# Kernel optimization log

Measured on AMD Instinct MI355X. Metric: run time of the kernel, lower is better.

Reference implementation:

```python
import jax, jax.numpy as jnp
import numpy as np

EPSILON = 0.1
NITER = 50


def _sinkhorn_transport(cost, epsilon, niter):
    # Faithful to the torch loop: kernel uses exp(-cost/eps), scalings have +100
    # damping, early-exit when both u,v L2 diffs < 0.01 (emulated via a done flag
    # inside a fixed-length scan so it is jit- and vjp-friendly).
    exp_term = jnp.exp(-cost / epsilon)              # [N, M]
    N, M = cost.shape
    u0 = jnp.ones((N, 1), cost.dtype)
    v0 = jnp.ones((M, 1), cost.dtype)

    def step(carry, _):
        u, v, pu, pv, done = carry
        nu = 1.0 / (exp_term @ v + 100.0)            # [N,1]
        nv = 1.0 / (exp_term.T @ nu + 100.0)         # [M,1]
        conv = (jnp.linalg.norm(nu - pu) < 0.01) & (jnp.linalg.norm(nv - pv) < 0.01)
        u_n = jnp.where(done, u, nu)
        v_n = jnp.where(done, v, nv)
        # torch updates prev only when the break was NOT taken this iteration
        pu_n = jnp.where(done | conv, pu, nu)
        pv_n = jnp.where(done | conv, pv, nv)
        return (u_n, v_n, pu_n, pv_n, done | conv), None

    (u, v, _, _, _), _ = jax.lax.scan(step, (u0, v0, u0, v0, jnp.array(False)), None, length=niter)
    # NOTE: original code uses exp(-cost * eps) here (not /eps); keep it faithful.
    return jnp.exp(-cost * epsilon) * u * v.T        # [N, M]


def _interp_lastdim(text, W):
    # PyTorch trilinear interpolate from (1,1,N) -> (D,H,W), align_corners=False.
    # Size-1 depth/height dims reduce to broadcast; only last dim is linear.
    B, C, N = text.shape
    scale = N / W
    x = jnp.maximum((jnp.arange(W, dtype=text.dtype) + 0.5) * scale - 0.5, 0.0)
    x0 = jnp.clip(jnp.floor(x).astype(jnp.int32), 0, N - 1)
    x1 = jnp.minimum(x0 + 1, N - 1)
    w = x - x0.astype(text.dtype)
    return text[:, :, x0] * (1.0 - w) + text[:, :, x1] * w   # [B, C, W]


def _forward(text, image, w1, b1, w2, b2):
    B, C, N = text.shape
    _, _, D, H, W = image.shape
    M = D * H * W
    tf = text.reshape(B * C, N)                      # [L, N]
    imf = image.reshape(B * C, M)                    # [L, M]
    A = tf.T                                         # [N, L]
    Bm = imf.T                                       # [M, L]
    d2 = (jnp.sum(A * A, axis=1)[:, None]
          + jnp.sum(Bm * Bm, axis=1)[None, :]
          - 2.0 * (A @ Bm.T))
    cost = jnp.sqrt(jnp.maximum(d2, 0.0))            # torch.cdist p=2, [N, M]
    T = _sinkhorn_transport(cost, EPSILON, NITER)
    aligned_text = (imf @ T.T).reshape(B, C, N)      # [B, C, N]

    t_line = _interp_lastdim(aligned_text, W)        # [B, C, W]
    t_rs = jnp.broadcast_to(t_line[:, :, None, None, :], (B, C, D, H, W))
    fused = jnp.concatenate([t_rs, image], axis=1)   # [B, 2C, D, H, W]

    h = jnp.einsum('oi,bidhw->bodhw', w1, fused) + b1[None, :, None, None, None]
    h = jax.nn.relu(h)
    g = jnp.einsum('oi,bidhw->bodhw', w2, h) + b2[None, :, None, None, None]
    gate = jax.nn.sigmoid(g)
    return image * (1.0 - gate) + t_rs * gate


def setup_inputs() -> dict:
    key = jax.random.key(0)
    ks = jax.random.split(key, 6)
    B, C, N = 2, 64, 256
    D, H, W = 32, 64, 64
    return {
        'text': jax.random.normal(ks[0], (B, C, N), dtype=jnp.float32),
        'image': jax.random.normal(ks[1], (B, C, D, H, W), dtype=jnp.float32),
        'w1': jax.random.normal(ks[2], (C, 2 * C), dtype=jnp.float32) * (1.0 / np.sqrt(2 * C)),
        'b1': jax.random.normal(ks[3], (C,), dtype=jnp.float32) * 0.01,
        'w2': jax.random.normal(ks[4], (C, C), dtype=jnp.float32) * (1.0 / np.sqrt(C)),
        'b2': jax.random.normal(ks[5], (C,), dtype=jnp.float32) * 0.01,
    }


def reference(text, image, w1, b1, w2, b2):
    return _forward(text, image, w1, b1, w2, b2)
```

## Files before the change

### kernel.cpp

```cpp
#include <hip/hip_runtime.h>

#define L_ 128
#define N_ 256
#define M_ 131072

using short8  = __attribute__((ext_vector_type(8)))  short;
using floatx16 = __attribute__((ext_vector_type(16))) float;

__device__ __forceinline__ unsigned short f2bf(float f) {
  unsigned u = __float_as_uint(f);
  u += 0x7fffu + ((u >> 16) & 1u);
  return (unsigned short)(u >> 16);
}
__device__ __forceinline__ float bf2f(unsigned short s) {
  return __uint_as_float(((unsigned)s) << 16);
}
__device__ __forceinline__ unsigned pack2(float x, float y) {
  return ((unsigned)f2bf(y) << 16) | (unsigned)f2bf(x);
}
__device__ __forceinline__ floatx16 mm(uint4 a, uint4 b, floatx16 c) {
  return __builtin_amdgcn_mfma_f32_32x32x16_bf16(
      __builtin_bit_cast(short8, a), __builtin_bit_cast(short8, b), c, 0, 0, 0);
}

__global__ __launch_bounds__(256, 2) void k_gemm(
    const float* __restrict__ image, const float* __restrict__ text,
    unsigned* __restrict__ imf_Tp, unsigned short* __restrict__ pbuf) {
  __shared__ unsigned SH[13952];
  float* SHf = (float*)SH;
  unsigned* v1 = SH;
  unsigned* uu = SH + 4608;
  unsigned short* w16 = (unsigned short*)(SH + 8960);
  const int t = threadIdx.x;
  const int lane = t & 63, w = t >> 6;
  const int q = lane >> 5, r = lane & 31;
  const int wnu = w >> 1, wm = w & 1;
  const int wl = w >> 1, wn = w & 1;
  const int m_base = blockIdx.x * 256;

  {
    const int nuh = t & 127, half = t >> 7;
    const int n = 4 * (nuh >> 1) + 1 + (nuh & 1);
    float sq = 0.f;
#pragma unroll 8
    for (int j = 0; j < 32; ++j) {
      const int l0 = half * 64 + 2 * j;
      const float x = text[l0 * N_ + n];
      const float y = text[(l0 + 1) * N_ + n];
      sq = fmaf(x, x, fmaf(y, y, sq));
      SH[nuh * 64 + half * 32 + j] = pack2(x, y);
    }
    ((float*)w16)[nuh * 2 + half] = sq;
  }
  __syncthreads();
  uint4 at[2][8];
#pragma unroll
  for (int nt = 0; nt < 2; ++nt)
#pragma unroll
    for (int kk = 0; kk < 8; ++kk)
      at[nt][kk] = *(const uint4*)&SH[(wnu * 64 + nt * 32 + r) * 64 + kk * 8 + q * 4];
  if (t < 128)
    SHf[13824 + t] = ((float*)w16)[t * 2] + ((float*)w16)[t * 2 + 1];

  floatx16 zz;
#pragma unroll
  for (int i = 0; i < 16; ++i) zz[i] = 0.f;
  floatx16 acc2[2][2] = {zz, zz, zz, zz};

  const int rowg = t >> 4;
  const int mqi = t & 15;
  const int mq = mqi * 4;

  for (int s = 0; s < 4; ++s) {
    const int msub = m_base + s * 64;
    __syncthreads();
    float sq0 = 0.f, sq1 = 0.f, sq2 = 0.f, sq3 = 0.f;
#pragma unroll
    for (int i = 0; i < 8; ++i) {
      const int l = rowg + 16 * i;
      const float4 v = *(const float4*)&image[(size_t)l * M_ + msub + mq];
      sq0 = fmaf(v.x, v.x, sq0);
      sq1 = fmaf(v.y, v.y, sq1);
      sq2 = fmaf(v.z, v.z, sq2);
      sq3 = fmaf(v.w, v.w, sq3);
      uint2 pr; pr.x = pack2(v.x, v.y); pr.y = pack2(v.z, v.w);
      *(uint2*)&v1[l * 36 + (mq >> 1)] = pr;
    }
    sq0 += __shfl_xor(sq0, 16); sq0 += __shfl_xor(sq0, 32);
    sq1 += __shfl_xor(sq1, 16); sq1 += __shfl_xor(sq1, 32);
    sq2 += __shfl_xor(sq2, 16); sq2 += __shfl_xor(sq2, 32);
    sq3 += __shfl_xor(sq3, 16); sq3 += __shfl_xor(sq3, 32);
    if (lane < 16) {
      SHf[13568 + w * 64 + mq + 0] = sq0;
      SHf[13568 + w * 64 + mq + 1] = sq1;
      SHf[13568 + w * 64 + mq + 2] = sq2;
      SHf[13568 + w * 64 + mq + 3] = sq3;
    }
    __syncthreads();
    {
      const int m = t & 63;
      const bool modd = (m & 1) != 0;
#pragma unroll
      for (int j = 0; j < 16; ++j) {
        const int lp = w * 16 + j;
        const unsigned a = v1[(2 * lp) * 36 + (m >> 1)];
        const unsigned c = v1[(2 * lp + 1) * 36 + (m >> 1)];
        uu[m * 68 + lp] = modd ? ((a >> 16) | (c & 0xffff0000u))
                               : ((a & 0xffffu) | (c << 16));
      }
    }
    __syncthreads();
#pragma unroll
    for (int i = 0; i < 8; ++i) {
      const int m = i * 8 + (t >> 5);
      const int p = t & 31;
      const uint2 o = *(const uint2*)&uu[m * 68 + 2 * p];
      *(uint2*)&imf_Tp[(size_t)(msub + m) * 64 + 2 * p] = o;
    }
    floatx16 acc1[2] = {zz, zz};
#pragma unroll
    for (int kk = 0; kk < 8; ++kk) {
      const uint4 bv = *(const uint4*)&uu[(wm * 32 + r) * 68 + kk * 8 + q * 4];
      acc1[0] = mm(at[0][kk], bv, acc1[0]);
      acc1[1] = mm(at[1][kk], bv, acc1[1]);
    }
    const int mloc = wm * 32 + r;
    const float bn = SHf[13568 + mloc] + SHf[13568 + 64 + mloc] +
                     SHf[13568 + 128 + mloc] + SHf[13568 + 192 + mloc];
#pragma unroll
    for (int nt = 0; nt < 2; ++nt)
#pragma unroll
      for (int reg = 0; reg < 16; ++reg) {
        const int nu = wnu * 64 + nt * 32 + (reg & 3) + 8 * (reg >> 2) + 4 * q;
        const float d2 = SHf[13824 + nu] + bn - 2.0f * acc1[nt][reg];
        const float cst = sqrtf(fmaxf(d2, 0.0f));
        w16[nu * 72 + mloc] = f2bf(__expf(-0.1f * cst) * 1e-4f);
      }
    __syncthreads();
#pragma unroll
    for (int kk2 = 0; kk2 < 4; ++kk2) {
      const uint4 a0 = *(const uint4*)&v1[(wl * 64 + r) * 36 + kk2 * 8 + q * 4];
      const uint4 a1 = *(const uint4*)&v1[(wl * 64 + 32 + r) * 36 + kk2 * 8 + q * 4];
      const uint4 b0 = *(const uint4*)&((unsigned*)w16)[(wn * 64 + r) * 36 + kk2 * 8 + q * 4];
      const uint4 b1 = *(const uint4*)&((unsigned*)w16)[(wn * 64 + 32 + r) * 36 + kk2 * 8 + q * 4];
      acc2[0][0] = mm(a0, b0, acc2[0][0]);
      acc2[0][1] = mm(a0, b1, acc2[0][1]);
      acc2[1][0] = mm(a1, b0, acc2[1][0]);
      acc2[1][1] = mm(a1, b1, acc2[1][1]);
    }
  }
#pragma unroll
  for (int lt = 0; lt < 2; ++lt)
#pragma unroll
    for (int nt2 = 0; nt2 < 2; ++nt2)
#pragma unroll
      for (int reg = 0; reg < 16; ++reg) {
        const int l = wl * 64 + lt * 32 + (reg & 3) + 8 * (reg >> 2) + 4 * q;
        const int nu = wn * 64 + nt2 * 32 + r;
        pbuf[((size_t)blockIdx.x * 128 + l) * 128 + nu] = f2bf(acc2[lt][nt2][reg]);
      }
}

__global__ __launch_bounds__(256) void k_tline(const unsigned short* __restrict__ pbuf,
                                               float* __restrict__ tline) {
  __shared__ float red[2][4][64];
  const int t = threadIdx.x;
  const int l = blockIdx.x;
  const int j = t & 63, part = t >> 6;
  float s1 = 0.f, s2 = 0.f;
  for (int b = part; b < 512; b += 4) {
    const unsigned v = *(const unsigned*)&pbuf[((size_t)b * 128 + l) * 128 + 2 * j];
    s1 += bf2f((unsigned short)(v & 0xffffu));
    s2 += bf2f((unsigned short)(v >> 16));
  }
  red[0][part][j] = s1; red[1][part][j] = s2;
  __syncthreads();
  if (t < 64) {
    float S1 = 0.f, S2 = 0.f;
#pragma unroll
    for (int p = 0; p < 4; ++p) { S1 += red[0][p][t]; S2 += red[1][p][t]; }
    tline[l * 64 + t] = S1 * 0.5f + S2 * 0.5f;
  }
}

__global__ __launch_bounds__(256) void k_fuse2(
    const unsigned* __restrict__ imf_Tp, const float* __restrict__ w1,
    const float* __restrict__ b1, const float* __restrict__ w2,
    const float* __restrict__ b2, const float* __restrict__ tline,
    float* __restrict__ out) {
  __shared__ float P1T[64 * 66];
  __shared__ float TLT[64 * 66];
  __shared__ unsigned hb[4 * 32 * 34];
  __shared__ float b2s[64];
  const int t = threadIdx.x;
  const int lane = t & 63, wv = t >> 6;
  const int q = lane >> 5, r = lane & 31;
  const int b = blockIdx.x >> 8;
  const int chunk = blockIdx.x & 255;
  unsigned* __restrict__ hbw = hb + wv * (32 * 34);

  for (int i = t; i < 4096; i += 256) {
    const int c = i >> 6, ww = i & 63;
    TLT[ww * 66 + c] = tline[b * 4096 + i];
  }
  if (t < 64) b2s[t] = b2[t];

  uint4 w1f[2][4], w2f[2][4];
#pragma unroll
  for (int ct = 0; ct < 2; ++ct)
#pragma unroll
    for (int s = 0; s < 4; ++s) {
      const int kp0 = s * 8 + q * 4;
      const float* w1r = w1 + (ct * 32 + r) * 128 + 64 + 2 * kp0;
      const float* w2r = w2 + (ct * 32 + r) * 64 + 2 * kp0;
      float2 u0 = *(const float2*)(w1r + 0), u1 = *(const float2*)(w1r + 2);
      float2 u2 = *(const float2*)(w1r + 4), u3 = *(const float2*)(w1r + 6);
      uint4 f1; f1.x = pack2(u0.x, u0.y); f1.y = pack2(u1.x, u1.y);
      f1.z = pack2(u2.x, u2.y); f1.w = pack2(u3.x, u3.y);
      w1f[ct][s] = f1;
      u0 = *(const float2*)(w2r + 0); u1 = *(const float2*)(w2r + 2);
      u2 = *(const float2*)(w2r + 4); u3 = *(const float2*)(w2r + 6);
      uint4 f2; f2.x = pack2(u0.x, u0.y); f2.y = pack2(u1.x, u1.y);
      f2.z = pack2(u2.x, u2.y); f2.w = pack2(u3.x, u3.y);
      w2f[ct][s] = f2;
    }
  __syncthreads();
  {
    const int ww = t & 63;
#pragma unroll
    for (int og = 0; og < 16; ++og) {
      const int o = (t >> 6) * 16 + og;
      float acc = b1[o];
      const float* w1r = w1 + o * 128;
#pragma unroll 8
      for (int c = 0; c < 64; ++c) acc = fmaf(w1r[c], TLT[ww * 66 + c], acc);
      P1T[ww * 66 + o] = acc;
    }
  }

  floatx16 zz;
#pragma unroll
  for (int i = 0; i < 16; ++i) zz[i] = 0.f;

  for (int pass = 0; pass < 4; ++pass) {
    const int mbase = chunk * 512 + pass * 128 + wv * 32;
    const int m = mbase + r;
    const int ww = m & 63;
    floatx16 d1[2] = {zz, zz};
#pragma unroll
    for (int s = 0; s < 4; ++s) {
      const uint4 bfr = *(const uint4*)&imf_Tp[(size_t)m * 64 + b * 32 + s * 8 + q * 4];
      d1[0] = mm(w1f[0][s], bfr, d1[0]);
      d1[1] = mm(w1f[1][s], bfr, d1[1]);
    }
    __syncthreads();
#pragma unroll
    for (int ct = 0; ct < 2; ++ct)
#pragma unroll
      for (int R = 0; R < 4; ++R) {
        const int cb = ct * 32 + 8 * R + 4 * q;
        const float2 pa = *(const float2*)&P1T[ww * 66 + cb];
        const float2 pb = *(const float2*)&P1T[ww * 66 + cb + 2];
        const float h0 = fmaxf(d1[ct][R * 4 + 0] + pa.x, 0.f);
        const float h1 = fmaxf(d1[ct][R * 4 + 1] + pa.y, 0.f);
        const float h2 = fmaxf(d1[ct][R * 4 + 2] + pb.x, 0.f);
        const float h3 = fmaxf(d1[ct][R * 4 + 3] + pb.y, 0.f);
        const int kp0 = ct * 16 + 4 * R + 2 * q;
        uint2 pr; pr.x = pack2(h0, h1); pr.y = pack2(h2, h3);
        *(uint2*)&hbw[r * 34 + kp0] = pr;
      }
    __syncthreads();
    floatx16 d2[2] = {zz, zz};
#pragma unroll
    for (int s = 0; s < 4; ++s) {
      const uint2 hlo = *(const uint2*)&hbw[r * 34 + s * 8 + q * 4];
      const uint2 hhi = *(const uint2*)&hbw[r * 34 + s * 8 + q * 4 + 2];
      uint4 bfr2; bfr2.x = hlo.x; bfr2.y = hlo.y; bfr2.z = hhi.x; bfr2.w = hhi.y;
      d2[0] = mm(w2f[0][s], bfr2, d2[0]);
      d2[1] = mm(w2f[1][s], bfr2, d2[1]);
    }
#pragma unroll
    for (int ot = 0; ot < 2; ++ot)
#pragma unroll
      for (int R = 0; R < 4; ++R) {
        const int ob = ot * 32 + 8 * R + 4 * q;
        const float2 ta = *(const float2*)&TLT[ww * 66 + ob];
        const float2 tb = *(const float2*)&TLT[ww * 66 + ob + 2];
        const float trs[4] = {ta.x, ta.y, tb.x, tb.y};
        const unsigned iv01 = imf_Tp[(size_t)m * 64 + b * 32 + (ob >> 1)];
        const unsigned iv23 = imf_Tp[(size_t)m * 64 + b * 32 + (ob >> 1) + 1];
        const float ivv[4] = {
            bf2f((unsigned short)(iv01 & 0xffffu)),
            bf2f((unsigned short)(iv01 >> 16)),
            bf2f((unsigned short)(iv23 & 0xffffu)),
            bf2f((unsigned short)(iv23 >> 16))};
#pragma unroll
        for (int j = 0; j < 4; ++j) {
          const int o = ob + j;
          const float g = d2[ot][R * 4 + j] + b2s[o];
          const float gate = 1.0f / (1.0f + __expf(-g));
          const size_t gidx = (size_t)(b * 64 + o) * M_ + m;
          out[gidx] = fmaf(gate, trs[j] - ivv[j], ivv[j]);
        }
      }
  }
}

extern "C" void kernel_launch(void* const* d_in, const int* in_sizes, int n_in,
                              void* d_out, int out_size, void* d_ws, size_t ws_size,
                              hipStream_t stream) {
  const float* text  = (const float*)d_in[0];
  const float* image = (const float*)d_in[1];
  const float* w1    = (const float*)d_in[2];
  const float* b1    = (const float*)d_in[3];
  const float* w2    = (const float*)d_in[4];
  const float* b2    = (const float*)d_in[5];
  float* out = (float*)d_out;

  char* ws = (char*)d_ws;
  unsigned short* pbuf = (unsigned short*)(ws);
  unsigned* imf_Tp  = (unsigned*)(ws + 33554432);
  float*    tline   = (float*)(ws + 67666432);

  k_gemm <<<512,  256, 0, stream>>>(image, text, imf_Tp, pbuf);
  k_tline<<<128,  256, 0, stream>>>(pbuf, tline);
  k_fuse2<<<512,  256, 0, stream>>>(imf_Tp, w1, b1, w2, b2, tline, out);
}
```

Baseline: 230.7 us.

## Reblock bf16 image buffer for coalesced loads, use MFMA for text projection

```diff
diff --git a/kernel.cpp b/kernel.cpp
--- a/kernel.cpp
+++ b/kernel.cpp
@@ -25,7 +25,7 @@
 
 __global__ __launch_bounds__(256, 2) void k_gemm(
     const float* __restrict__ image, const float* __restrict__ text,
-    unsigned* __restrict__ imf_Tp, unsigned short* __restrict__ pbuf) {
+    unsigned* __restrict__ imf2, unsigned short* __restrict__ pbuf) {
   __shared__ unsigned SH[13952];
   float* SHf = (float*)SH;
   unsigned* v1 = SH;
@@ -68,8 +68,7 @@
   floatx16 acc2[2][2] = {zz, zz, zz, zz};
 
   const int rowg = t >> 4;
-  const int mqi = t & 15;
-  const int mq = mqi * 4;
+  const int mq = (t & 15) * 4;
 
   for (int s = 0; s < 4; ++s) {
     const int msub = m_base + s * 64;
@@ -111,11 +110,11 @@
     }
     __syncthreads();
 #pragma unroll
-    for (int i = 0; i < 8; ++i) {
-      const int m = i * 8 + (t >> 5);
-      const int p = t & 31;
-      const uint2 o = *(const uint2*)&uu[m * 68 + 2 * p];
-      *(uint2*)&imf_Tp[(size_t)(msub + m) * 64 + 2 * p] = o;
+    for (int i = 0; i < 4; ++i) {
+      const int idx = t + 256 * i;
+      const int bkq = idx >> 6, m = idx & 63;
+      const uint4 v = *(const uint4*)&uu[m * 68 + bkq * 4];
+      *(uint4*)&imf2[((size_t)((unsigned)bkq << 17) + msub + m) * 4] = v;
     }
     floatx16 acc1[2] = {zz, zz};
 #pragma unroll
@@ -183,15 +182,15 @@
   }
 }
 
-__global__ __launch_bounds__(256) void k_fuse2(
-    const unsigned* __restrict__ imf_Tp, const float* __restrict__ w1,
+__global__ __launch_bounds__(256, 3) void k_fuse2(
+    const unsigned* __restrict__ imf2, const float* __restrict__ w1,
     const float* __restrict__ b1, const float* __restrict__ w2,
     const float* __restrict__ b2, const float* __restrict__ tline,
     float* __restrict__ out) {
   __shared__ float P1T[64 * 66];
   __shared__ float TLT[64 * 66];
   __shared__ unsigned hb[4 * 32 * 34];
-  __shared__ float b2s[64];
+  __shared__ float b1s[64], b2s[64];
   const int t = threadIdx.x;
   const int lane = t & 63, wv = t >> 6;
   const int q = lane >> 5, r = lane & 31;
@@ -203,7 +202,7 @@
     const int c = i >> 6, ww = i & 63;
     TLT[ww * 66 + c] = tline[b * 4096 + i];
   }
-  if (t < 64) b2s[t] = b2[t];
+  if (t < 64) { b1s[t] = b1[t]; b2s[t] = b2[t]; }
 
   uint4 w1f[2][4], w2f[2][4];
 #pragma unroll
@@ -225,18 +224,39 @@
       w2f[ct][s] = f2;
     }
   __syncthreads();
+
   {
-    const int ww = t & 63;
-#pragma unroll
-    for (int og = 0; og < 16; ++og) {
-      const int o = (t >> 6) * 16 + og;
-      float acc = b1[o];
-      const float* w1r = w1 + o * 128;
-#pragma unroll 8
-      for (int c = 0; c < 64; ++c) acc = fmaf(w1r[c], TLT[ww * 66 + c], acc);
-      P1T[ww * 66 + o] = acc;
-    }
-  }
+    const int ot2 = wv & 1, wt = wv >> 1;
+    uint4 aF[4], bF[4];
+#pragma unroll
+    for (int s = 0; s < 4; ++s) {
+      const int kp0 = s * 8 + q * 4;
+      const float* w1r = w1 + (ot2 * 32 + r) * 128 + 2 * kp0;
+      float2 u0 = *(const float2*)(w1r + 0), u1 = *(const float2*)(w1r + 2);
+      float2 u2 = *(const float2*)(w1r + 4), u3 = *(const float2*)(w1r + 6);
+      uint4 f; f.x = pack2(u0.x, u0.y); f.y = pack2(u1.x, u1.y);
+      f.z = pack2(u2.x, u2.y); f.w = pack2(u3.x, u3.y);
+      aF[s] = f;
+      const float* tl = &TLT[(wt * 32 + r) * 66 + 2 * kp0];
+      float2 v0 = *(const float2*)(tl + 0), v1_ = *(const float2*)(tl + 2);
+      float2 v2 = *(const float2*)(tl + 4), v3 = *(const float2*)(tl + 6);
+      uint4 g; g.x = pack2(v0.x, v0.y); g.y = pack2(v1_.x, v1_.y);
+      g.z = pack2(v2.x, v2.y); g.w = pack2(v3.x, v3.y);
+      bF[s] = g;
+    }
+    floatx16 p1a;
+#pragma unroll
+    for (int reg = 0; reg < 16; ++reg)
+      p1a[reg] = b1s[ot2 * 32 + (reg & 3) + 8 * (reg >> 2) + 4 * q];
+#pragma unroll
+    for (int s = 0; s < 4; ++s) p1a = mm(aF[s], bF[s], p1a);
+#pragma unroll
+    for (int reg = 0; reg < 16; ++reg) {
+      const int o = ot2 * 32 + (reg & 3) + 8 * (reg >> 2) + 4 * q;
+      P1T[(wt * 32 + r) * 66 + o] = p1a[reg];
+    }
+  }
+  __syncthreads();
 
   floatx16 zz;
 #pragma unroll
@@ -249,11 +269,11 @@
     floatx16 d1[2] = {zz, zz};
 #pragma unroll
     for (int s = 0; s < 4; ++s) {
-      const uint4 bfr = *(const uint4*)&imf_Tp[(size_t)m * 64 + b * 32 + s * 8 + q * 4];
+      const uint4 bfr = *(const uint4*)&imf2[
+          ((size_t)((unsigned)(b * 8 + s * 2 + q) << 17) + m) * 4];
       d1[0] = mm(w1f[0][s], bfr, d1[0]);
       d1[1] = mm(w1f[1][s], bfr, d1[1]);
     }
-    __syncthreads();
 #pragma unroll
     for (int ct = 0; ct < 2; ++ct)
 #pragma unroll
@@ -269,7 +289,6 @@
         uint2 pr; pr.x = pack2(h0, h1); pr.y = pack2(h2, h3);
         *(uint2*)&hbw[r * 34 + kp0] = pr;
       }
-    __syncthreads();
     floatx16 d2[2] = {zz, zz};
 #pragma unroll
     for (int s = 0; s < 4; ++s) {
@@ -287,13 +306,13 @@
         const float2 ta = *(const float2*)&TLT[ww * 66 + ob];
         const float2 tb = *(const float2*)&TLT[ww * 66 + ob + 2];
         const float trs[4] = {ta.x, ta.y, tb.x, tb.y};
-        const unsigned iv01 = imf_Tp[(size_t)m * 64 + b * 32 + (ob >> 1)];
-        const unsigned iv23 = imf_Tp[(size_t)m * 64 + b * 32 + (ob >> 1) + 1];
+        const uint2 iv = *(const uint2*)&imf2[
+            ((size_t)((unsigned)(b * 8 + ot * 4 + R) << 17) + m) * 4 + 2 * q];
         const float ivv[4] = {
-            bf2f((unsigned short)(iv01 & 0xffffu)),
-            bf2f((unsigned short)(iv01 >> 16)),
-            bf2f((unsigned short)(iv23 & 0xffffu)),
-            bf2f((unsigned short)(iv23 >> 16))};
+            bf2f((unsigned short)(iv.x & 0xffffu)),
+            bf2f((unsigned short)(iv.x >> 16)),
+            bf2f((unsigned short)(iv.y & 0xffffu)),
+            bf2f((unsigned short)(iv.y >> 16))};
 #pragma unroll
         for (int j = 0; j < 4; ++j) {
           const int o = ob + j;
@@ -319,10 +338,10 @@
 
   char* ws = (char*)d_ws;
   unsigned short* pbuf = (unsigned short*)(ws);
-  unsigned* imf_Tp  = (unsigned*)(ws + 33554432);
+  unsigned* imf2    = (unsigned*)(ws + 33554432);
   float*    tline   = (float*)(ws + 67666432);
 
-  k_gemm <<<512,  256, 0, stream>>>(image, text, imf_Tp, pbuf);
+  k_gemm <<<512,  256, 0, stream>>>(image, text, imf2, pbuf);
   k_tline<<<128,  256, 0, stream>>>(pbuf, tline);
-  k_fuse2<<<512,  256, 0, stream>>>(imf_Tp, w1, b1, w2, b2, tline, out);
-}
+  k_fuse2<<<512,  256, 0, stream>>>(imf2, w1, b1, w2, b2, tline, out);
+}
```

New measurement: 243.0 us. 5.3% more time.
